# Kernel tuning notes

Hardware: AMD Instinct MI355X
Metric: run time of the kernel (lower is better)

Reference implementation:

```python
import jax, jax.numpy as jnp
import numpy as np

B, L, D = 4, 4096, 128
WINDOW = 64
NEG = -1e9
LN_EPS = 1e-5


def setup_inputs() -> dict:
    key = jax.random.key(0)
    ks = jax.random.split(key, 6)
    x = jax.random.normal(ks[0], (B, L, D), dtype=jnp.float32)
    # windowed adjacency with self-loops: adj[b,i,j]=1 iff |i-j| <= WINDOW
    idx = jnp.arange(L)
    band = (jnp.abs(idx[:, None] - idx[None, :]) <= WINDOW).astype(jnp.int32)
    adj = jnp.broadcast_to(band, (B, L, L))
    mask = np.ones((B, L), dtype=np.int32)
    mask[B // 2 :, -L // 8 :] = 0
    mask = jnp.asarray(mask)
    s = 1.0 / np.sqrt(D)
    Wq = jax.random.normal(ks[1], (D, D), dtype=jnp.float32) * s
    Wk = jax.random.normal(ks[2], (D, D), dtype=jnp.float32) * s
    Wv = jax.random.normal(ks[3], (D, D), dtype=jnp.float32) * s
    W_upd = jax.random.normal(ks[4], (2 * D, D), dtype=jnp.float32) * (1.0 / np.sqrt(2 * D))
    b_upd = jnp.zeros((D,), dtype=jnp.float32)
    gamma = jnp.ones((D,), dtype=jnp.float32)
    beta = jnp.zeros((D,), dtype=jnp.float32)
    return {"x": x, "adj": adj, "mask": mask, "Wq": Wq, "Wk": Wk, "Wv": Wv,
            "W_upd": W_upd, "b_upd": b_upd, "gamma": gamma, "beta": beta}


def reference(x, adj, mask, Wq, Wk, Wv, W_upd, b_upd, gamma, beta):
    d = x.shape[-1]
    q = jnp.einsum("bld,de->ble", x, Wq)
    k = jnp.einsum("bld,de->ble", x, Wk)
    v = jnp.einsum("bld,de->ble", x, Wv)
    logits = jnp.einsum("bld,bmd->blm", q, k) / jnp.sqrt(jnp.float32(d))
    logits = jnp.where(adj == 0, NEG, logits)
    logits = jnp.where(mask[:, :, None] == 0, NEG, logits)
    logits = jnp.where(mask[:, None, :] == 0, NEG, logits)
    attn = jax.nn.softmax(logits, axis=-1)  # dropout = identity (eval mode)
    agg = jnp.einsum("blm,bmd->bld", attn, v)
    h = jnp.concatenate([x, agg], axis=-1)  # [B, L, 2D]
    upd = jax.nn.relu(h @ W_upd + b_upd)
    y = x + upd
    mu = jnp.mean(y, axis=-1, keepdims=True)
    var = jnp.var(y, axis=-1, keepdims=True)
    return gamma * (y - mu) * jax.lax.rsqrt(var + LN_EPS) + beta
```

## Files before the change

### kernel.cpp

```cpp
#include <hip/hip_runtime.h>

#define BB 4
#define LL 4096
#define DD 128
#define WIN 64
#define BL (BB * LL)

typedef unsigned short u16;
using bf16x8 = __attribute__((ext_vector_type(8))) short;
using f32x4 = __attribute__((ext_vector_type(4))) float;

__device__ __forceinline__ u16 f2b(float f) {
  union { float f; unsigned int u; } x;
  x.f = f;
  unsigned int r = x.u + 0x7fffu + ((x.u >> 16) & 1u);
  return (u16)(r >> 16);
}
__device__ __forceinline__ float b2f_lo(unsigned int u) {
  union { unsigned int u; float f; } x;
  x.u = u << 16;
  return x.f;
}
__device__ __forceinline__ float b2f_hi(unsigned int u) {
  union { unsigned int u; float f; } x;
  x.u = u & 0xffff0000u;
  return x.f;
}
__device__ __forceinline__ void unpack8(uint4 u, float* f) {
  f[0] = b2f_lo(u.x); f[1] = b2f_hi(u.x);
  f[2] = b2f_lo(u.y); f[3] = b2f_hi(u.y);
  f[4] = b2f_lo(u.z); f[5] = b2f_hi(u.z);
  f[6] = b2f_lo(u.w); f[7] = b2f_hi(u.w);
}
__device__ __forceinline__ float comp4(float4 a, int d) {
  return d == 0 ? a.x : (d == 1 ? a.y : (d == 2 ? a.z : a.w));
}

__global__ __launch_bounds__(256) void qkv_kernel(
    const float* __restrict__ x, const float* __restrict__ Wq,
    const float* __restrict__ Wk, const float* __restrict__ Wv,
    const float* __restrict__ Wu, u16* __restrict__ q, u16* __restrict__ k,
    u16* __restrict__ v, float* __restrict__ vmean_sum,
    u16* __restrict__ Wut) {
  __shared__ float xs[64][132];

  const int t = threadIdx.x;
  const int which = blockIdx.y;

  if (which == 3) {
    if (blockIdx.x < 128) {
      int idx = blockIdx.x * 256 + t;
      int n = idx >> 8;
      int kd = idx & 255;
      Wut[n * 256 + kd] = f2b(Wu[kd * 128 + n]);
    }
    return;
  }

  const int row0 = blockIdx.x * 64;
  const float* __restrict__ W = which == 0 ? Wq : (which == 1 ? Wk : Wv);
  u16* __restrict__ outp = which == 0 ? q : (which == 1 ? k : v);

  {
    const float4* xg = (const float4*)(x + (size_t)row0 * DD);
    #pragma unroll
    for (int p = 0; p < 8; ++p) {
      int idx = t + 256 * p;
      ((float4*)&xs[idx >> 5][0])[idx & 31] = xg[idx];
    }
  }
  __syncthreads();

  const int rg = t >> 5;
  const int cg = t & 31;
  const float4* W4 = (const float4*)W;

  float4 acc[8];
  #pragma unroll
  for (int m = 0; m < 8; ++m) acc[m] = make_float4(0.f, 0.f, 0.f, 0.f);

  #pragma unroll 2
  for (int k4 = 0; k4 < 32; ++k4) {
    float4 a[8];
    #pragma unroll
    for (int m = 0; m < 8; ++m)
      a[m] = ((const float4*)&xs[rg + 8 * m][0])[k4];
    #pragma unroll
    for (int d = 0; d < 4; ++d) {
      float4 w = W4[(size_t)(k4 * 4 + d) * 32 + cg];
      #pragma unroll
      for (int m = 0; m < 8; ++m) {
        float av = comp4(a[m], d);
        acc[m].x += av * w.x; acc[m].y += av * w.y;
        acc[m].z += av * w.z; acc[m].w += av * w.w;
      }
    }
  }

  #pragma unroll
  for (int m = 0; m < 8; ++m) {
    ushort4 s;
    s.x = f2b(acc[m].x); s.y = f2b(acc[m].y);
    s.z = f2b(acc[m].z); s.w = f2b(acc[m].w);
    *(ushort4*)(outp + (size_t)(row0 + rg + 8 * m) * DD + 4 * cg) = s;
  }

  if (which == 2) {
    __syncthreads();
    float4 cs = make_float4(0.f, 0.f, 0.f, 0.f);
    #pragma unroll
    for (int m = 0; m < 8; ++m) {
      cs.x += acc[m].x; cs.y += acc[m].y; cs.z += acc[m].z; cs.w += acc[m].w;
    }
    ((float4*)&xs[rg][0])[cg] = cs;
    __syncthreads();
    if (t < DD) {
      float s = 0.f;
      #pragma unroll
      for (int r = 0; r < 8; ++r) s += xs[r][t];
      atomicAdd(&vmean_sum[(row0 >> 12) * DD + t], s);
    }
  }
}

struct SA {
  u16 qs[32][136];
  u16 ks[64][136];
  u16 vs[64][136];
  float pt[64][36];
};
struct SM {
  u16 hs[32][264];
  float ys[32][132];
};
union SU { SA a; SM m; };

__global__ __launch_bounds__(256) void attn_mlp_kernel(
    const u16* __restrict__ q, const u16* __restrict__ k,
    const u16* __restrict__ v, const float* __restrict__ vmean_sum,
    const int* __restrict__ mask, const float* __restrict__ x,
    const u16* __restrict__ Wut, const float* __restrict__ bias,
    const float* __restrict__ gamma, const float* __restrict__ beta,
    float* __restrict__ out) {
  __shared__ __align__(16) SU sm;
  __shared__ int cms[64];
  __shared__ float rowsum[32];
  __shared__ float lsumw[4][32];

  const int bx = blockIdx.x;
  const int b = bx >> 7;
  const int i0 = (bx & 127) * 32;
  const int t = threadIdx.x;
  const int tm = t >> 4;
  const int tn = t & 15;
  const int w = t >> 6;
  const int lane = t & 63;
  const int quad = lane >> 4;
  const int l16 = lane & 15;
  const size_t rowbase = ((size_t)b * LL + i0) * DD;
  const f32x4 zero4 = {0.f, 0.f, 0.f, 0.f};

  {
    const uint4* qg = (const uint4*)(q + rowbase);
    #pragma unroll
    for (int p = 0; p < 2; ++p) {
      int idx = t + 256 * p;
      *(uint4*)&sm.a.qs[idx >> 4][8 * (idx & 15)] = qg[idx];
    }
  }

  float accv[2][8];
  #pragma unroll
  for (int r = 0; r < 2; ++r)
    #pragma unroll
    for (int j = 0; j < 8; ++j) accv[r][j] = 0.f;
  float lsumA[2][4] = {{0.f, 0.f, 0.f, 0.f}, {0.f, 0.f, 0.f, 0.f}};

  for (int ch = 0; ch < 3; ++ch) {
    const int j0 = i0 - WIN + ch * 64;
    __syncthreads();

    {
      const uint4* kg = (const uint4*)(k + (size_t)b * LL * DD);
      const uint4* vg = (const uint4*)(v + (size_t)b * LL * DD);
      #pragma unroll
      for (int p = 0; p < 4; ++p) {
        int idx = t + 256 * p;
        int row = idx >> 4, c = idx & 15;
        int j = j0 + row;
        int jc = j < 0 ? 0 : (j > LL - 1 ? LL - 1 : j);
        *(uint4*)&sm.a.ks[row][8 * c] = kg[(size_t)jc * 16 + c];
        *(uint4*)&sm.a.vs[row][8 * c] = vg[(size_t)jc * 16 + c];
      }
      if (t < 64) {
        int j = j0 + t;
        cms[t] = (j >= 0 && j < LL) ? mask[b * LL + j] : 0;
      }
    }
    __syncthreads();

    f32x4 S[2];
    S[0] = zero4; S[1] = zero4;
    #pragma unroll
    for (int k0 = 0; k0 < 4; ++k0) {
      bf16x8 bk = *(const bf16x8*)&sm.a.ks[w * 16 + l16][32 * k0 + 8 * quad];
      #pragma unroll
      for (int mt = 0; mt < 2; ++mt) {
        bf16x8 aq =
            *(const bf16x8*)&sm.a.qs[mt * 16 + l16][32 * k0 + 8 * quad];
        S[mt] = __builtin_amdgcn_mfma_f32_16x16x32_bf16(aq, bk, S[mt], 0, 0, 0);
      }
    }

    {
      const int col = w * 16 + l16;
      const int j = j0 + col;
      const bool okc = ((unsigned)j < (unsigned)LL) && (cms[col] != 0);
      #pragma unroll
      for (int mt = 0; mt < 2; ++mt) {
        #pragma unroll
        for (int r = 0; r < 4; ++r) {
          int row = mt * 16 + quad * 4 + r;
          int dj = (i0 + row) - j;
          dj = dj < 0 ? -dj : dj;
          float p = (okc && dj <= WIN)
                        ? __expf(S[mt][r] * 0.08838834764831845f)
                        : 0.f;
          lsumA[mt][r] += p;
          sm.a.pt[col][row] = p;
        }
      }
    }
    __syncthreads();

    #pragma unroll 2
    for (int c = 0; c < 64; ++c) {
      float2 pv = *(const float2*)&sm.a.pt[c][2 * tm];
      float vf[8];
      unpack8(*(const uint4*)&sm.a.vs[c][8 * tn], vf);
      #pragma unroll
      for (int j = 0; j < 8; ++j) {
        accv[0][j] += pv.x * vf[j];
        accv[1][j] += pv.y * vf[j];
      }
    }
  }

  #pragma unroll
  for (int mt = 0; mt < 2; ++mt) {
    #pragma unroll
    for (int r = 0; r < 4; ++r) {
      float s = lsumA[mt][r];
      s += __shfl_xor(s, 1);
      s += __shfl_xor(s, 2);
      s += __shfl_xor(s, 4);
      s += __shfl_xor(s, 8);
      if (l16 == 0) lsumw[w][mt * 16 + quad * 4 + r] = s;
    }
  }
  __syncthreads();

  if (t < 32)
    rowsum[t] = lsumw[0][t] + lsumw[1][t] + lsumw[2][t] + lsumw[3][t];
  {
    const float4* xg = (const float4*)(x + rowbase);
    #pragma unroll
    for (int p = 0; p < 4; ++p) {
      int idx = t + 256 * p;
      int row = idx >> 5, c4 = idx & 31;
      float4 xv = xg[row * 32 + c4];
      ushort4 pk;
      pk.x = f2b(xv.x); pk.y = f2b(xv.y); pk.z = f2b(xv.z); pk.w = f2b(xv.w);
      *(ushort4*)&sm.m.hs[row][4 * c4] = pk;
    }
  }
  __syncthreads();

  #pragma unroll
  for (int r = 0; r < 2; ++r) {
    int row = 2 * tm + r;
    float inv = 1.0f / rowsum[row];
    float o[8];
    if (mask[b * LL + i0 + row] != 0) {
      #pragma unroll
      for (int j = 0; j < 8; ++j) o[j] = accv[r][j] * inv;
    } else {
      const float s = 1.0f / LL;
      #pragma unroll
      for (int j = 0; j < 8; ++j) o[j] = vmean_sum[b * DD + 8 * tn + j] * s;
    }
    ushort4 pk;
    pk.x = f2b(o[0]); pk.y = f2b(o[1]); pk.z = f2b(o[2]); pk.w = f2b(o[3]);
    *(ushort4*)&sm.m.hs[row][DD + 8 * tn] = pk;
    pk.x = f2b(o[4]); pk.y = f2b(o[5]); pk.z = f2b(o[6]); pk.w = f2b(o[7]);
    *(ushort4*)&sm.m.hs[row][DD + 8 * tn + 4] = pk;
  }
  __syncthreads();

  f32x4 upd[2][2];
  upd[0][0] = zero4; upd[0][1] = zero4;
  upd[1][0] = zero4; upd[1][1] = zero4;
  #pragma unroll 2
  for (int ks8 = 0; ks8 < 8; ++ks8) {
    bf16x8 ah[2];
    #pragma unroll
    for (int mt = 0; mt < 2; ++mt)
      ah[mt] = *(const bf16x8*)&sm.m.hs[mt * 16 + l16][32 * ks8 + 8 * quad];
    #pragma unroll
    for (int ntl = 0; ntl < 2; ++ntl) {
      int n = (2 * w + ntl) * 16 + l16;
      bf16x8 bw = *(const bf16x8*)&Wut[(size_t)n * 256 + 32 * ks8 + 8 * quad];
      #pragma unroll
      for (int mt = 0; mt < 2; ++mt)
        upd[mt][ntl] = __builtin_amdgcn_mfma_f32_16x16x32_bf16(
            ah[mt], bw, upd[mt][ntl], 0, 0, 0);
    }
  }

  #pragma unroll
  for (int mt = 0; mt < 2; ++mt) {
    #pragma unroll
    for (int ntl = 0; ntl < 2; ++ntl) {
      int dim = (2 * w + ntl) * 16 + l16;
      float bv = bias[dim];
      #pragma unroll
      for (int r = 0; r < 4; ++r) {
        int row = mt * 16 + quad * 4 + r;
        float u = upd[mt][ntl][r] + bv;
        u = u > 0.f ? u : 0.f;
        sm.m.ys[row][dim] = x[rowbase + (size_t)row * DD + dim] + u;
      }
    }
  }
  __syncthreads();

  {
    const int row = t >> 3, sg = t & 7;
    float4 yv[4];
    float s = 0.f, ss = 0.f;
    #pragma unroll
    for (int i = 0; i < 4; ++i) {
      yv[i] = *(const float4*)&sm.m.ys[row][16 * sg + 4 * i];
      s += yv[i].x + yv[i].y + yv[i].z + yv[i].w;
      ss += yv[i].x * yv[i].x + yv[i].y * yv[i].y + yv[i].z * yv[i].z +
            yv[i].w * yv[i].w;
    }
    s += __shfl_xor(s, 1); ss += __shfl_xor(ss, 1);
    s += __shfl_xor(s, 2); ss += __shfl_xor(ss, 2);
    s += __shfl_xor(s, 4); ss += __shfl_xor(ss, 4);
    float mu = s * (1.0f / DD);
    float var = ss * (1.0f / DD) - mu * mu;
    float rstd = rsqrtf(var + 1e-5f);
    float* op = out + rowbase + (size_t)row * DD;
    #pragma unroll
    for (int i = 0; i < 4; ++i) {
      int d0 = 16 * sg + 4 * i;
      float4 g = *(const float4*)&gamma[d0];
      float4 be = *(const float4*)&beta[d0];
      float4 o;
      o.x = g.x * ((yv[i].x - mu) * rstd) + be.x;
      o.y = g.y * ((yv[i].y - mu) * rstd) + be.y;
      o.z = g.z * ((yv[i].z - mu) * rstd) + be.z;
      o.w = g.w * ((yv[i].w - mu) * rstd) + be.w;
      *(float4*)&op[d0] = o;
    }
  }
}

extern "C" void kernel_launch(void* const* d_in, const int* in_sizes, int n_in,
                              void* d_out, int out_size, void* d_ws,
                              size_t ws_size, hipStream_t stream) {
  const float* x = (const float*)d_in[0];
  const int* mask = (const int*)d_in[2];
  const float* Wq = (const float*)d_in[3];
  const float* Wk = (const float*)d_in[4];
  const float* Wv = (const float*)d_in[5];
  const float* Wu = (const float*)d_in[6];
  const float* bias = (const float*)d_in[7];
  const float* gamma = (const float*)d_in[8];
  const float* beta = (const float*)d_in[9];
  float* out = (float*)d_out;

  u16* q = (u16*)d_ws;
  u16* k = q + (size_t)BL * DD;
  u16* v = k + (size_t)BL * DD;
  float* vmean_sum = (float*)(v + (size_t)BL * DD);
  u16* Wut = (u16*)(vmean_sum + BB * DD);

  hipMemsetAsync(vmean_sum, 0, BB * DD * sizeof(float), stream);

  qkv_kernel<<<dim3(BL / 64, 4), 256, 0, stream>>>(x, Wq, Wk, Wv, Wu, q, k, v,
                                                   vmean_sum, Wut);
  attn_mlp_kernel<<<BL / 32, 256, 0, stream>>>(q, k, v, vmean_sum, mask, x,
                                               Wut, bias, gamma, beta, out);
}
```

Baseline: 366.8 us.

## Use bf16 MFMA for QKV projection with pre-transposed bf16 weights

Replaces the scalar fp32 FMA projection in the QKV kernel with bf16 MFMA 16x16x32 instructions. x is converted to bf16 in shared memory, and a separate small kernel transposes and converts Wq/Wk/Wv/Wu into one bf16 buffer. The V column sums for the mean are now reduced with shuffles instead of shared memory. This adds one kernel launch and rounds x and the weights to bf16, which lowers precision, and the output stores become scalar 2-byte writes.

```diff
diff --git a/kernel.cpp b/kernel.cpp
--- a/kernel.cpp
+++ b/kernel.cpp
@@ -32,93 +32,120 @@
   f[4] = b2f_lo(u.z); f[5] = b2f_hi(u.z);
   f[6] = b2f_lo(u.w); f[7] = b2f_hi(u.w);
 }
-__device__ __forceinline__ float comp4(float4 a, int d) {
-  return d == 0 ? a.x : (d == 1 ? a.y : (d == 2 ? a.z : a.w));
+
+#define WT_TOTAL 81920
+#define WUT_OFF 49152
+
+__global__ __launch_bounds__(256) void wt_kernel(
+    const float* __restrict__ Wq, const float* __restrict__ Wk,
+    const float* __restrict__ Wv, const float* __restrict__ Wu,
+    u16* __restrict__ WT) {
+  int idx = blockIdx.x * 512 + 2 * threadIdx.x;
+  if (idx >= WT_TOTAL) return;
+  #pragma unroll
+  for (int e = 0; e < 2; ++e) {
+    int id = idx + e;
+    u16 val;
+    if (id < WUT_OFF) {
+      int wsel = id >> 14;
+      int r = id & 16383;
+      int n = r >> 7, kd = r & 127;
+      const float* Wsrc = wsel == 0 ? Wq : (wsel == 1 ? Wk : Wv);
+      val = f2b(Wsrc[kd * 128 + n]);
+    } else {
+      int r = id - WUT_OFF;
+      int n = r >> 8, kd = r & 255;
+      val = f2b(Wu[kd * 128 + n]);
+    }
+    WT[id] = val;
+  }
 }
 
 __global__ __launch_bounds__(256) void qkv_kernel(
-    const float* __restrict__ x, const float* __restrict__ Wq,
-    const float* __restrict__ Wk, const float* __restrict__ Wv,
-    const float* __restrict__ Wu, u16* __restrict__ q, u16* __restrict__ k,
+    const float* __restrict__ x, u16* __restrict__ q, u16* __restrict__ k,
     u16* __restrict__ v, float* __restrict__ vmean_sum,
-    u16* __restrict__ Wut) {
-  __shared__ float xs[64][132];
+    const u16* __restrict__ WT) {
+  __shared__ u16 xs[64][136];
 
   const int t = threadIdx.x;
   const int which = blockIdx.y;
-
-  if (which == 3) {
-    if (blockIdx.x < 128) {
-      int idx = blockIdx.x * 256 + t;
-      int n = idx >> 8;
-      int kd = idx & 255;
-      Wut[n * 256 + kd] = f2b(Wu[kd * 128 + n]);
-    }
-    return;
-  }
-
   const int row0 = blockIdx.x * 64;
-  const float* __restrict__ W = which == 0 ? Wq : (which == 1 ? Wk : Wv);
   u16* __restrict__ outp = which == 0 ? q : (which == 1 ? k : v);
+  const u16* __restrict__ WTb = WT + which * 16384;
 
   {
     const float4* xg = (const float4*)(x + (size_t)row0 * DD);
     #pragma unroll
     for (int p = 0; p < 8; ++p) {
       int idx = t + 256 * p;
-      ((float4*)&xs[idx >> 5][0])[idx & 31] = xg[idx];
+      int row = idx >> 5, c4 = idx & 31;
+      float4 xv = xg[idx];
+      ushort4 pk;
+      pk.x = f2b(xv.x); pk.y = f2b(xv.y); pk.z = f2b(xv.z); pk.w = f2b(xv.w);
+      *(ushort4*)&xs[row][4 * c4] = pk;
     }
   }
   __syncthreads();
 
-  const int rg = t >> 5;
-  const int cg = t & 31;
-  const float4* W4 = (const float4*)W;
-
-  float4 acc[8];
-  #pragma unroll
-  for (int m = 0; m < 8; ++m) acc[m] = make_float4(0.f, 0.f, 0.f, 0.f);
-
-  #pragma unroll 2
-  for (int k4 = 0; k4 < 32; ++k4) {
-    float4 a[8];
-    #pragma unroll
-    for (int m = 0; m < 8; ++m)
-      a[m] = ((const float4*)&xs[rg + 8 * m][0])[k4];
-    #pragma unroll
-    for (int d = 0; d < 4; ++d) {
-      float4 w = W4[(size_t)(k4 * 4 + d) * 32 + cg];
-      #pragma unroll
-      for (int m = 0; m < 8; ++m) {
-        float av = comp4(a[m], d);
-        acc[m].x += av * w.x; acc[m].y += av * w.y;
-        acc[m].z += av * w.z; acc[m].w += av * w.w;
-      }
-    }
-  }
-
-  #pragma unroll
-  for (int m = 0; m < 8; ++m) {
-    ushort4 s;
-    s.x = f2b(acc[m].x); s.y = f2b(acc[m].y);
-    s.z = f2b(acc[m].z); s.w = f2b(acc[m].w);
-    *(ushort4*)(outp + (size_t)(row0 + rg + 8 * m) * DD + 4 * cg) = s;
+  const int w = t >> 6;
+  const int lane = t & 63;
+  const int quad = lane >> 4;
+  const int l16 = lane & 15;
+  const f32x4 zero4 = {0.f, 0.f, 0.f, 0.f};
+
+  f32x4 acc[4][2];
+  #pragma unroll
+  for (int mt = 0; mt < 4; ++mt) {
+    acc[mt][0] = zero4;
+    acc[mt][1] = zero4;
+  }
+
+  #pragma unroll
+  for (int k0 = 0; k0 < 4; ++k0) {
+    bf16x8 bw[2];
+    #pragma unroll
+    for (int ntl = 0; ntl < 2; ++ntl) {
+      int n = (2 * w + ntl) * 16 + l16;
+      bw[ntl] = *(const bf16x8*)&WTb[(size_t)n * 128 + 32 * k0 + 8 * quad];
+    }
+    #pragma unroll
+    for (int mt = 0; mt < 4; ++mt) {
+      bf16x8 aq = *(const bf16x8*)&xs[mt * 16 + l16][32 * k0 + 8 * quad];
+      #pragma unroll
+      for (int ntl = 0; ntl < 2; ++ntl)
+        acc[mt][ntl] = __builtin_amdgcn_mfma_f32_16x16x32_bf16(
+            aq, bw[ntl], acc[mt][ntl], 0, 0, 0);
+    }
+  }
+
+  u16* op = outp + (size_t)row0 * DD;
+  #pragma unroll
+  for (int mt = 0; mt < 4; ++mt) {
+    #pragma unroll
+    for (int ntl = 0; ntl < 2; ++ntl) {
+      int col = (2 * w + ntl) * 16 + l16;
+      #pragma unroll
+      for (int r = 0; r < 4; ++r) {
+        int row = mt * 16 + quad * 4 + r;
+        op[(size_t)row * DD + col] = f2b(acc[mt][ntl][r]);
+      }
+    }
   }
 
   if (which == 2) {
-    __syncthreads();
-    float4 cs = make_float4(0.f, 0.f, 0.f, 0.f);
-    #pragma unroll
-    for (int m = 0; m < 8; ++m) {
-      cs.x += acc[m].x; cs.y += acc[m].y; cs.z += acc[m].z; cs.w += acc[m].w;
-    }
-    ((float4*)&xs[rg][0])[cg] = cs;
-    __syncthreads();
-    if (t < DD) {
-      float s = 0.f;
-      #pragma unroll
-      for (int r = 0; r < 8; ++r) s += xs[r][t];
-      atomicAdd(&vmean_sum[(row0 >> 12) * DD + t], s);
+    #pragma unroll
+    for (int ntl = 0; ntl < 2; ++ntl) {
+      float cs = 0.f;
+      #pragma unroll
+      for (int mt = 0; mt < 4; ++mt)
+        #pragma unroll
+        for (int r = 0; r < 4; ++r) cs += acc[mt][ntl][r];
+      cs += __shfl_xor(cs, 16);
+      cs += __shfl_xor(cs, 32);
+      if (quad == 0) {
+        int col = (2 * w + ntl) * 16 + l16;
+        atomicAdd(&vmean_sum[(row0 >> 12) * DD + col], cs);
+      }
     }
   }
 }
@@ -385,12 +412,13 @@
   u16* k = q + (size_t)BL * DD;
   u16* v = k + (size_t)BL * DD;
   float* vmean_sum = (float*)(v + (size_t)BL * DD);
-  u16* Wut = (u16*)(vmean_sum + BB * DD);
+  u16* WT = (u16*)(vmean_sum + BB * DD);
 
   hipMemsetAsync(vmean_sum, 0, BB * DD * sizeof(float), stream);
 
-  qkv_kernel<<<dim3(BL / 64, 4), 256, 0, stream>>>(x, Wq, Wk, Wv, Wu, q, k, v,
-                                                   vmean_sum, Wut);
+  wt_kernel<<<160, 256, 0, stream>>>(Wq, Wk, Wv, Wu, WT);
+  qkv_kernel<<<dim3(BL / 64, 3), 256, 0, stream>>>(x, q, k, v, vmean_sum, WT);
   attn_mlp_kernel<<<BL / 32, 256, 0, stream>>>(q, k, v, vmean_sum, mask, x,
-                                               Wut, bias, gamma, beta, out);
-}
+                                               WT + WUT_OFF, bias, gamma, beta,
+                                               out);
+}
```

Result: faster. 354.4 us (-3.4%).
